# Performance work log

Measured on AMD Instinct MI355X. Metric: run time of the kernel, lower is better.

The kernel has to match this reference:

```python
import jax, jax.numpy as jnp
import numpy as np

B, N, E = 64, 256, 2048          # graphs per batch, nodes per subgraph, edges per subgraph
V, D, H = 50000, 128, 4          # vocab_size, hidden_dim, heads
NEG_SLOPE = 0.2                  # PyG GATConv default LeakyReLU slope


def setup_inputs() -> dict:
    key = jax.random.key(0)
    ks = jax.random.split(key, 16)
    s = 0.05
    return {
        "neighbors_node1": jax.random.randint(ks[0], (B, N), 0, V),
        "neighbors_node2": jax.random.randint(ks[1], (B, N), 0, V),
        "adj1": jax.random.randint(ks[2], (B, 2, E), 0, N),
        "adj2": jax.random.randint(ks[3], (B, 2, E), 0, N),
        "emb": jax.random.normal(ks[4], (V + 1, D), jnp.float32) * 0.02,
        # GATConv 1: lin weight [H*D, D], att_src/att_dst [H, D], bias [D] (concat=False)
        "W1": jax.random.normal(ks[5], (H * D, D), jnp.float32) * s,
        "att_src1": jax.random.normal(ks[6], (H, D), jnp.float32) * s,
        "att_dst1": jax.random.normal(ks[7], (H, D), jnp.float32) * s,
        "b1": jnp.zeros((D,), jnp.float32),
        # GATConv 2
        "W2": jax.random.normal(ks[8], (H * D, D), jnp.float32) * s,
        "att_src2": jax.random.normal(ks[9], (H, D), jnp.float32) * s,
        "att_dst2": jax.random.normal(ks[10], (H, D), jnp.float32) * s,
        "b2": jnp.zeros((D,), jnp.float32),
        # final MLP: Linear(2D -> 1)
        "mlp_w": jax.random.normal(ks[11], (1, 2 * D), jnp.float32) * s,
        "mlp_b": jnp.zeros((1,), jnp.float32),
    }


def _gat_conv(x, edge_index, W, a_src, a_dst, bias):
    """PyG GATConv, concat=False (mean over heads), with self-loops.
    x: [N, D] node features; edge_index: [2, E] (row=src j, col=dst i)."""
    xh = (x @ W.T).reshape(N, H, D)                      # [N, H, D]
    loop = jnp.arange(N)
    src = jnp.concatenate([edge_index[0], loop])          # [E+N]
    dst = jnp.concatenate([edge_index[1], loop])
    asrc = jnp.einsum('nhd,hd->nh', xh, a_src)            # [N, H]
    adst = jnp.einsum('nhd,hd->nh', xh, a_dst)
    e = jax.nn.leaky_relu(asrc[src] + adst[dst], NEG_SLOPE)   # [E+N, H]
    # softmax over incoming edges of each dst node
    m = jax.ops.segment_max(e, dst, num_segments=N)
    ex = jnp.exp(e - m[dst])
    denom = jax.ops.segment_sum(ex, dst, num_segments=N)
    alpha = ex / denom[dst]                               # [E+N, H]
    out = jax.ops.segment_sum(xh[src] * alpha[:, :, None], dst, num_segments=N)  # [N, H, D]
    return out.mean(axis=1) + bias                        # [N, D]


def reference(neighbors_node1, neighbors_node2, adj1, adj2, emb,
              W1, att_src1, att_dst1, b1,
              W2, att_src2, att_dst2, b2,
              mlp_w, mlp_b):
    f1 = jax.vmap(lambda n, ei: _gat_conv(emb[n], ei, W1, att_src1, att_dst1, b1))(
        neighbors_node1, adj1)                            # [B, N, D]
    f2 = jax.vmap(lambda n, ei: _gat_conv(emb[n], ei, W2, att_src2, att_dst2, b2))(
        neighbors_node2, adj2)
    feats = jnp.concatenate([f1[:, 0], f2[:, 0]], axis=-1)  # center node of each subgraph -> [B, 2D]
    return (feats @ mlp_w.T + mlp_b)[:, 0]                # [B]
```

## Files before the change

### kernel.cpp

```cpp
#include <hip/hip_runtime.h>
#include <hip/hip_bf16.h>

#define Bg 64
#define Nn 256
#define Ee 2048
#define Dd 128
#define Hh 4
#define MAXJ 40
#define RS 132

__device__ __forceinline__ float bf2f(unsigned short u) {
    return __uint_as_float(((unsigned)u) << 16);
}

__global__ __launch_bounds__(256) void precompute_kernel(
    const void* W1, const void* as1, const void* ad1, const void* b1,
    const void* W2, const void* as2, const void* ad2, const void* b2,
    const void* mlpw, const void* mlpb, float* wv)
{
    __shared__ float s_av[3 * Dd];
    __shared__ float s_part[8 * 3 * Dd];
    __shared__ float s_red[2];
    __shared__ int   s_f32;

    const int tid = threadIdx.x;
    const int x = blockIdx.x;
    const int l = x >> 2, h = x & 3;

    if (tid < 64) {
        float v = bf2f(((const unsigned short*)W1)[tid]);
        bool bad = !(v > -64.f && v < 64.f);
        unsigned long long m = __ballot(bad);
        if (tid == 0) s_f32 = (m != 0ull) ? 1 : 0;
    }
    __syncthreads();
    const int f32 = s_f32;

    for (int i = tid; i < 3 * Dd; i += 256) {
        int t = i >> 7, d = i & 127;
        const void* p; long off;
        if (t == 0)      { p = l ? as2 : as1; off = (long)h * Dd + d; }
        else if (t == 1) { p = l ? ad2 : ad1; off = (long)h * Dd + d; }
        else             { p = mlpw;          off = (long)l * Dd + d; }
        s_av[i] = f32 ? ((const float*)p)[off]
                      : bf2f(((const unsigned short*)p)[off]);
    }
    __syncthreads();

    {
        const int kc = (tid & 31) * 4;
        const int d0 = (tid >> 5) * 16;
        float acc[3][4] = {};
        if (f32) {
            const float* Wf = (const float*)(l ? W2 : W1) + (long)h * Dd * Dd;
            #pragma unroll
            for (int dd = 0; dd < 16; ++dd) {
                int d = d0 + dd;
                float4 w = *(const float4*)(Wf + (long)d * Dd + kc);
                #pragma unroll
                for (int t = 0; t < 3; ++t) {
                    float a = s_av[t * Dd + d];
                    acc[t][0] += a * w.x; acc[t][1] += a * w.y;
                    acc[t][2] += a * w.z; acc[t][3] += a * w.w;
                }
            }
        } else {
            const unsigned short* Wb =
                (const unsigned short*)(l ? W2 : W1) + (long)h * Dd * Dd;
            #pragma unroll
            for (int dd = 0; dd < 16; ++dd) {
                int d = d0 + dd;
                ushort4 u = *(const ushort4*)(Wb + (long)d * Dd + kc);
                float wx = bf2f(u.x), wy = bf2f(u.y);
                float wz = bf2f(u.z), ww = bf2f(u.w);
                #pragma unroll
                for (int t = 0; t < 3; ++t) {
                    float a = s_av[t * Dd + d];
                    acc[t][0] += a * wx; acc[t][1] += a * wy;
                    acc[t][2] += a * wz; acc[t][3] += a * ww;
                }
            }
        }
        const int dg = tid >> 5;
        #pragma unroll
        for (int t = 0; t < 3; ++t)
            *(float4*)&s_part[(dg * 3 + t) * Dd + kc] =
                make_float4(acc[t][0], acc[t][1], acc[t][2], acc[t][3]);
    }
    __syncthreads();

    for (int i = tid; i < 3 * Dd; i += 256) {
        int t = i >> 7, k = i & 127;
        float s = 0.f;
        #pragma unroll
        for (int g = 0; g < 8; ++g) s += s_part[(g * 3 + t) * Dd + k];
        wv[((l * 3 + t) * 4 + h) * Dd + k] = s;
    }

    if (h == 0) {
        float p = 0.f;
        if (tid < 128) {
            const void* bias = l ? b2 : b1;
            float bv = f32 ? ((const float*)bias)[tid]
                           : bf2f(((const unsigned short*)bias)[tid]);
            p = bv * s_av[2 * Dd + tid];
        }
        #pragma unroll
        for (int off = 32; off > 0; off >>= 1) p += __shfl_down(p, off);
        if (tid == 0 || tid == 64) s_red[tid >> 6] = p;
        __syncthreads();
        if (tid == 0) {
            float a = s_red[0] + s_red[1];
            if (l == 0) a += f32 ? ((const float*)mlpb)[0]
                                 : bf2f(((const unsigned short*)mlpb)[0]);
            wv[3072 + l] = a;
        }
    }
}

__global__ __launch_bounds__(512) void gat_main_kernel(
    const int* nn1, const int* nn2, const int* adj1, const int* adj2,
    const void* emb, const void* W1, const float* wv, void* out)
{
    __shared__ float s_wv[24 * RS];
    __shared__ float s_rows[2 * MAXJ * RS];
    __shared__ int   s_nodes[2][Nn];
    __shared__ int   s_srcj[2][MAXJ];
    __shared__ int   s_gid[2 * MAXJ];
    __shared__ int   s_cnt[2];
    __shared__ int   s_f32;
    __shared__ float s_ps[2 * MAXJ * Hh], s_pm[2 * MAXJ * Hh];
    __shared__ float s_pd[2 * Hh], s_hval[2 * Hh], s_bdot[2];

    const int tid = threadIdx.x;
    const int b = blockIdx.x;

    if (tid == 0) { s_cnt[0] = 0; s_cnt[1] = 0; }
    if (tid < 64) {
        float v = bf2f(((const unsigned short*)W1)[tid]);
        bool bad = !(v > -64.f && v < 64.f);
        unsigned long long m = __ballot(bad);
        if (tid == 0) s_f32 = (m != 0ull) ? 1 : 0;
    }
    __syncthreads();
    const int f32 = s_f32;

    for (int v = tid; v < 2 * (Ee / 4); v += 512) {
        int l = v >> 9, i = v & 511;
        const int* adjp = (l ? adj2 : adj1) + (long)b * 2 * Ee;
        int4 d4 = ((const int4*)(adjp + Ee))[i];
        int base = i * 4;
        if (d4.x == 0) { int p = atomicAdd(&s_cnt[l], 1); if (p < MAXJ - 1) s_srcj[l][p] = adjp[base + 0]; }
        if (d4.y == 0) { int p = atomicAdd(&s_cnt[l], 1); if (p < MAXJ - 1) s_srcj[l][p] = adjp[base + 1]; }
        if (d4.z == 0) { int p = atomicAdd(&s_cnt[l], 1); if (p < MAXJ - 1) s_srcj[l][p] = adjp[base + 2]; }
        if (d4.w == 0) { int p = atomicAdd(&s_cnt[l], 1); if (p < MAXJ - 1) s_srcj[l][p] = adjp[base + 3]; }
    }
    {
        int l = tid >> 8, n = tid & 255;
        s_nodes[l][n] = (l ? nn2 : nn1)[b * Nn + n];
    }
    for (int i = tid; i < 768; i += 512) {
        float4 f = ((const float4*)wv)[i];
        int el = i * 4, row = el >> 7, k = el & 127;
        *(float4*)&s_wv[row * RS + k] = f;
    }
    if (tid < 2) s_bdot[tid] = wv[3072 + tid];
    __syncthreads();

    if (tid < 2) {
        int c = s_cnt[tid];
        if (c > MAXJ - 1) c = MAXJ - 1;
        s_srcj[tid][c] = 0;
        s_cnt[tid] = c + 1;
    }
    __syncthreads();
    const int cnt0 = s_cnt[0], cnt1 = s_cnt[1];
    const int tot = cnt0 + cnt1;

    if (tid < 2 * MAXJ) {
        int l = tid / MAXJ, j = tid % MAXJ;
        int cl = l ? cnt1 : cnt0;
        if (j < cl) s_gid[l ? (cnt0 + j) : j] = s_nodes[l][s_srcj[l][j]];
    }
    __syncthreads();

    if (f32) {
        for (int idx = tid; idx < tot * 32; idx += 512) {
            int j = idx >> 5, k4 = (idx & 31) << 2;
            long gid = s_gid[j];
            float4 f = ((const float4*)emb)[gid * 32 + (k4 >> 2)];
            *(float4*)&s_rows[j * RS + k4] = f;
        }
    } else {
        for (int idx = tid; idx < tot * 16; idx += 512) {
            int j = idx >> 4, k8 = (idx & 15) << 3;
            long gid = s_gid[j];
            uint4 u = *(const uint4*)((const unsigned short*)emb + gid * Dd + k8);
            float4 f0 = make_float4(bf2f(u.x & 0xffff), bf2f(u.x >> 16),
                                    bf2f(u.y & 0xffff), bf2f(u.y >> 16));
            float4 f1 = make_float4(bf2f(u.z & 0xffff), bf2f(u.z >> 16),
                                    bf2f(u.w & 0xffff), bf2f(u.w >> 16));
            *(float4*)&s_rows[j * RS + k8] = f0;
            *(float4*)&s_rows[j * RS + k8 + 4] = f1;
        }
    }
    __syncthreads();

    const int ntask = tot * 8 + 8;
    for (int task = tid; task < ntask; task += 512) {
        int j, h, t, l;
        if (task < tot * 8) {
            j = task >> 3; h = (task >> 1) & 3; t = (task & 1) ? 2 : 0;
            l = (j < cnt0) ? 0 : 1;
        } else {
            int z = task - tot * 8;
            l = z >> 2; h = z & 3; t = 1;
            j = l ? (tot - 1) : (cnt0 - 1);
        }
        const float* wrow = s_wv + ((l * 3 + t) * 4 + h) * RS;
        const float* row  = s_rows + j * RS;
        float acc = 0.f;
        #pragma unroll 8
        for (int k = 0; k < Dd; ++k) acc += row[k] * wrow[k];
        if (task < tot * 8) {
            if (task & 1) s_pm[j * Hh + h] = acc;
            else          s_ps[j * Hh + h] = acc;
        } else {
            s_pd[(l << 2) | h] = acc;
        }
    }
    __syncthreads();

    if (tid < 8) {
        int l = tid >> 2, h = tid & 3;
        int j0 = l ? cnt0 : 0;
        int j1 = l ? tot : cnt0;
        float pd = s_pd[tid], m = -1e30f;
        for (int j = j0; j < j1; ++j) {
            float e = s_ps[j * Hh + h] + pd;
            e = (e >= 0.f) ? e : 0.2f * e;
            s_ps[j * Hh + h] = e;
            if (e > m) m = e;
        }
        float den = 0.f, num = 0.f;
        for (int j = j0; j < j1; ++j) {
            float ex = expf(s_ps[j * Hh + h] - m);
            den += ex;
            num += ex * s_pm[j * Hh + h];
        }
        s_hval[tid] = num / den;
    }
    __syncthreads();
    if (tid == 0) {
        float r = 0.25f * (s_hval[0] + s_hval[1] + s_hval[2] + s_hval[3]) + s_bdot[0]
                + 0.25f * (s_hval[4] + s_hval[5] + s_hval[6] + s_hval[7]) + s_bdot[1];
        if (f32) ((float*)out)[b] = r;
        else     ((__hip_bfloat16*)out)[b] = __float2bfloat16(r);
    }
}

extern "C" void kernel_launch(void* const* d_in, const int* in_sizes, int n_in,
                              void* d_out, int out_size, void* d_ws, size_t ws_size,
                              hipStream_t stream) {
    const int* nn1  = (const int*)d_in[0];
    const int* nn2  = (const int*)d_in[1];
    const int* adj1 = (const int*)d_in[2];
    const int* adj2 = (const int*)d_in[3];
    float* wv = (float*)d_ws;

    precompute_kernel<<<8, 256, 0, stream>>>(
        d_in[5],   d_in[6],   d_in[7],
        d_in[8],
        d_in[9],   d_in[10],  d_in[11],
        d_in[12],
        d_in[13],  d_in[14],  wv);

    gat_main_kernel<<<Bg, 512, 0, stream>>>(
        nn1, nn2, adj1, adj2, d_in[4] , d_in[5] , wv, d_out);
}
```

Measured before the change: 105.2 us.

## Fuse weight-projection precompute into main GAT kernel, recomputing per block

Removes the separate precompute kernel and has every block recompute the attention/MLP vector projections of W1/W2 itself, overlapping that work with the embedding gather. Adjacency loads are issued up front in a single pass per thread instead of in a loop. This drops one kernel launch and the workspace round trip. In exchange, each of the 64 blocks re-reads both full weight matrices (about 512KB) from L2 and does redundant FLOPs.

```diff
diff --git a/kernel.cpp b/kernel.cpp
--- a/kernel.cpp
+++ b/kernel.cpp
@@ -13,129 +13,43 @@
     return __uint_as_float(((unsigned)u) << 16);
 }
 
-__global__ __launch_bounds__(256) void precompute_kernel(
+__global__ __launch_bounds__(512) void gat_fused_kernel(
+    const int* nn1, const int* nn2, const int* adj1, const int* adj2,
+    const void* emb,
     const void* W1, const void* as1, const void* ad1, const void* b1,
     const void* W2, const void* as2, const void* ad2, const void* b2,
-    const void* mlpw, const void* mlpb, float* wv)
-{
-    __shared__ float s_av[3 * Dd];
-    __shared__ float s_part[8 * 3 * Dd];
-    __shared__ float s_red[2];
-    __shared__ int   s_f32;
-
-    const int tid = threadIdx.x;
-    const int x = blockIdx.x;
-    const int l = x >> 2, h = x & 3;
-
-    if (tid < 64) {
-        float v = bf2f(((const unsigned short*)W1)[tid]);
-        bool bad = !(v > -64.f && v < 64.f);
-        unsigned long long m = __ballot(bad);
-        if (tid == 0) s_f32 = (m != 0ull) ? 1 : 0;
-    }
-    __syncthreads();
-    const int f32 = s_f32;
-
-    for (int i = tid; i < 3 * Dd; i += 256) {
-        int t = i >> 7, d = i & 127;
-        const void* p; long off;
-        if (t == 0)      { p = l ? as2 : as1; off = (long)h * Dd + d; }
-        else if (t == 1) { p = l ? ad2 : ad1; off = (long)h * Dd + d; }
-        else             { p = mlpw;          off = (long)l * Dd + d; }
-        s_av[i] = f32 ? ((const float*)p)[off]
-                      : bf2f(((const unsigned short*)p)[off]);
-    }
-    __syncthreads();
-
-    {
-        const int kc = (tid & 31) * 4;
-        const int d0 = (tid >> 5) * 16;
-        float acc[3][4] = {};
-        if (f32) {
-            const float* Wf = (const float*)(l ? W2 : W1) + (long)h * Dd * Dd;
-            #pragma unroll
-            for (int dd = 0; dd < 16; ++dd) {
-                int d = d0 + dd;
-                float4 w = *(const float4*)(Wf + (long)d * Dd + kc);
-                #pragma unroll
-                for (int t = 0; t < 3; ++t) {
-                    float a = s_av[t * Dd + d];
-                    acc[t][0] += a * w.x; acc[t][1] += a * w.y;
-                    acc[t][2] += a * w.z; acc[t][3] += a * w.w;
-                }
-            }
-        } else {
-            const unsigned short* Wb =
-                (const unsigned short*)(l ? W2 : W1) + (long)h * Dd * Dd;
-            #pragma unroll
-            for (int dd = 0; dd < 16; ++dd) {
-                int d = d0 + dd;
-                ushort4 u = *(const ushort4*)(Wb + (long)d * Dd + kc);
-                float wx = bf2f(u.x), wy = bf2f(u.y);
-                float wz = bf2f(u.z), ww = bf2f(u.w);
-                #pragma unroll
-                for (int t = 0; t < 3; ++t) {
-                    float a = s_av[t * Dd + d];
-                    acc[t][0] += a * wx; acc[t][1] += a * wy;
-                    acc[t][2] += a * wz; acc[t][3] += a * ww;
-                }
-            }
-        }
-        const int dg = tid >> 5;
-        #pragma unroll
-        for (int t = 0; t < 3; ++t)
-            *(float4*)&s_part[(dg * 3 + t) * Dd + kc] =
-                make_float4(acc[t][0], acc[t][1], acc[t][2], acc[t][3]);
-    }
-    __syncthreads();
-
-    for (int i = tid; i < 3 * Dd; i += 256) {
-        int t = i >> 7, k = i & 127;
-        float s = 0.f;
-        #pragma unroll
-        for (int g = 0; g < 8; ++g) s += s_part[(g * 3 + t) * Dd + k];
-        wv[((l * 3 + t) * 4 + h) * Dd + k] = s;
-    }
-
-    if (h == 0) {
-        float p = 0.f;
-        if (tid < 128) {
-            const void* bias = l ? b2 : b1;
-            float bv = f32 ? ((const float*)bias)[tid]
-                           : bf2f(((const unsigned short*)bias)[tid]);
-            p = bv * s_av[2 * Dd + tid];
-        }
-        #pragma unroll
-        for (int off = 32; off > 0; off >>= 1) p += __shfl_down(p, off);
-        if (tid == 0 || tid == 64) s_red[tid >> 6] = p;
-        __syncthreads();
-        if (tid == 0) {
-            float a = s_red[0] + s_red[1];
-            if (l == 0) a += f32 ? ((const float*)mlpb)[0]
-                                 : bf2f(((const unsigned short*)mlpb)[0]);
-            wv[3072 + l] = a;
-        }
-    }
-}
-
-__global__ __launch_bounds__(512) void gat_main_kernel(
-    const int* nn1, const int* nn2, const int* adj1, const int* adj2,
-    const void* emb, const void* W1, const float* wv, void* out)
+    const void* mlpw, const void* mlpb, void* out)
 {
     __shared__ float s_wv[24 * RS];
     __shared__ float s_rows[2 * MAXJ * RS];
+    __shared__ float s_att[2 * 2 * Hh * Dd];
+    __shared__ float s_mlp[2 * Dd];
     __shared__ int   s_nodes[2][Nn];
     __shared__ int   s_srcj[2][MAXJ];
     __shared__ int   s_gid[2 * MAXJ];
     __shared__ int   s_cnt[2];
     __shared__ int   s_f32;
     __shared__ float s_ps[2 * MAXJ * Hh], s_pm[2 * MAXJ * Hh];
-    __shared__ float s_pd[2 * Hh], s_hval[2 * Hh], s_bdot[2];
+    __shared__ float s_pd[2 * Hh], s_hval[2 * Hh];
+    __shared__ float s_red4[4];
 
     const int tid = threadIdx.x;
     const int b = blockIdx.x;
 
-    if (tid == 0) { s_cnt[0] = 0; s_cnt[1] = 0; }
+    const int* adjp0 = adj1 + (long)b * 2 * Ee;
+    const int* adjp1 = adj2 + (long)b * 2 * Ee;
+    int4 d0 = ((const int4*)(adjp0 + Ee))[tid];
+    int4 s0 = ((const int4*)adjp0)[tid];
+    int4 d1 = ((const int4*)(adjp1 + Ee))[tid];
+    int4 s1 = ((const int4*)adjp1)[tid];
+
+    {
+        int l = tid >> 8, n = tid & 255;
+        s_nodes[l][n] = (l ? nn2 : nn1)[b * Nn + n];
+    }
+
+    if (tid < 2) s_cnt[tid] = 0;
+
     if (tid < 64) {
         float v = bf2f(((const unsigned short*)W1)[tid]);
         bool bad = !(v > -64.f && v < 64.f);
@@ -145,42 +59,68 @@
     __syncthreads();
     const int f32 = s_f32;
 
-    for (int v = tid; v < 2 * (Ee / 4); v += 512) {
-        int l = v >> 9, i = v & 511;
-        const int* adjp = (l ? adj2 : adj1) + (long)b * 2 * Ee;
-        int4 d4 = ((const int4*)(adjp + Ee))[i];
-        int base = i * 4;
-        if (d4.x == 0) { int p = atomicAdd(&s_cnt[l], 1); if (p < MAXJ - 1) s_srcj[l][p] = adjp[base + 0]; }
-        if (d4.y == 0) { int p = atomicAdd(&s_cnt[l], 1); if (p < MAXJ - 1) s_srcj[l][p] = adjp[base + 1]; }
-        if (d4.z == 0) { int p = atomicAdd(&s_cnt[l], 1); if (p < MAXJ - 1) s_srcj[l][p] = adjp[base + 2]; }
-        if (d4.w == 0) { int p = atomicAdd(&s_cnt[l], 1); if (p < MAXJ - 1) s_srcj[l][p] = adjp[base + 3]; }
-    }
     {
-        int l = tid >> 8, n = tid & 255;
-        s_nodes[l][n] = (l ? nn2 : nn1)[b * Nn + n];
-    }
-    for (int i = tid; i < 768; i += 512) {
-        float4 f = ((const float4*)wv)[i];
-        int el = i * 4, row = el >> 7, k = el & 127;
-        *(float4*)&s_wv[row * RS + k] = f;
-    }
-    if (tid < 2) s_bdot[tid] = wv[3072 + tid];
-    __syncthreads();
-
-    if (tid < 2) {
-        int c = s_cnt[tid];
-        if (c > MAXJ - 1) c = MAXJ - 1;
-        s_srcj[tid][c] = 0;
-        s_cnt[tid] = c + 1;
-    }
-    __syncthreads();
-    const int cnt0 = s_cnt[0], cnt1 = s_cnt[1];
-    const int tot = cnt0 + cnt1;
+        #define SCAN1(c, sv, l) \
+            if ((c) == 0) { int p = atomicAdd(&s_cnt[l], 1); \
+                            if (p < MAXJ - 1) s_srcj[l][p] = (sv); }
+        SCAN1(d0.x, s0.x, 0) SCAN1(d0.y, s0.y, 0)
+        SCAN1(d0.z, s0.z, 0) SCAN1(d0.w, s0.w, 0)
+        SCAN1(d1.x, s1.x, 1) SCAN1(d1.y, s1.y, 1)
+        SCAN1(d1.z, s1.z, 1) SCAN1(d1.w, s1.w, 1)
+        #undef SCAN1
+    }
+
+    for (int i = tid; i < 2304; i += 512) {
+        if (i < 2048) {
+            int l = i >> 10, t = (i >> 9) & 1, h = (i >> 7) & 3, d = i & 127;
+            const void* p = l ? (t ? ad2 : as2) : (t ? ad1 : as1);
+            long off = (long)h * Dd + d;
+            s_att[((l * 2 + t) * Hh + h) * Dd + d] =
+                f32 ? ((const float*)p)[off]
+                    : bf2f(((const unsigned short*)p)[off]);
+        } else {
+            int z = i - 2048, l = z >> 7, d = z & 127;
+            s_mlp[l * Dd + d] =
+                f32 ? ((const float*)mlpw)[l * Dd + d]
+                    : bf2f(((const unsigned short*)mlpw)[l * Dd + d]);
+        }
+    }
+
+    if (tid < 256) {
+        int l = tid >> 7, d = tid & 127;
+        const void* bp = l ? b2 : b1;
+        float bv = f32 ? ((const float*)bp)[d]
+                       : bf2f(((const unsigned short*)bp)[d]);
+        float mv = f32 ? ((const float*)mlpw)[l * Dd + d]
+                       : bf2f(((const unsigned short*)mlpw)[l * Dd + d]);
+        float p = bv * mv;
+        #pragma unroll
+        for (int off = 32; off > 0; off >>= 1) p += __shfl_down(p, off);
+        if ((tid & 63) == 0) s_red4[tid >> 6] = p;
+    }
+    __syncthreads();
+
+    float bd0 = 0.f, bd1 = 0.f;
+    if (tid == 0) {
+        bd0 = s_red4[0] + s_red4[1] +
+              (f32 ? ((const float*)mlpb)[0]
+                   : bf2f(((const unsigned short*)mlpb)[0]));
+        bd1 = s_red4[2] + s_red4[3];
+    }
+
+    int c0 = s_cnt[0]; if (c0 > MAXJ - 1) c0 = MAXJ - 1; c0 += 1;
+    int c1 = s_cnt[1]; if (c1 > MAXJ - 1) c1 = MAXJ - 1; c1 += 1;
+    const int tot = c0 + c1;
 
     if (tid < 2 * MAXJ) {
-        int l = tid / MAXJ, j = tid % MAXJ;
-        int cl = l ? cnt1 : cnt0;
-        if (j < cl) s_gid[l ? (cnt0 + j) : j] = s_nodes[l][s_srcj[l][j]];
+        int l = tid >= MAXJ;
+        int j = l ? tid - MAXJ : tid;
+        int cl = l ? c1 : c0;
+        int base = l ? c0 : 0;
+        if (j < cl) {
+            int src = (j == cl - 1) ? 0 : s_srcj[l][j];
+            s_gid[base + j] = s_nodes[l][src];
+        }
     }
     __syncthreads();
 
@@ -204,6 +144,42 @@
             *(float4*)&s_rows[j * RS + k8 + 4] = f1;
         }
     }
+
+    {
+        const int w = tid >> 6, lane = tid & 63;
+        const int l = w >> 2, h = w & 3;
+        const int k0 = lane * 2;
+        const float* av0 = s_att + ((l * 2 + 0) * Hh + h) * Dd;
+        const float* av1 = s_att + ((l * 2 + 1) * Hh + h) * Dd;
+        const float* av2 = s_mlp + l * Dd;
+        float a00 = 0.f, a01 = 0.f, a10 = 0.f, a11 = 0.f, a20 = 0.f, a21 = 0.f;
+        if (f32) {
+            const float* Wf = (const float*)(l ? W2 : W1) + (long)h * Dd * Dd;
+            #pragma unroll 8
+            for (int d = 0; d < Dd; ++d) {
+                float2 wr = *(const float2*)(Wf + (long)d * Dd + k0);
+                float x0 = av0[d], x1 = av1[d], x2 = av2[d];
+                a00 += x0 * wr.x; a01 += x0 * wr.y;
+                a10 += x1 * wr.x; a11 += x1 * wr.y;
+                a20 += x2 * wr.x; a21 += x2 * wr.y;
+            }
+        } else {
+            const unsigned short* Wb =
+                (const unsigned short*)(l ? W2 : W1) + (long)h * Dd * Dd;
+            #pragma unroll 8
+            for (int d = 0; d < Dd; ++d) {
+                unsigned u = *(const unsigned*)(Wb + (long)d * Dd + k0);
+                float wx = bf2f(u & 0xffff), wy = bf2f(u >> 16);
+                float x0 = av0[d], x1 = av1[d], x2 = av2[d];
+                a00 += x0 * wx; a01 += x0 * wy;
+                a10 += x1 * wx; a11 += x1 * wy;
+                a20 += x2 * wx; a21 += x2 * wy;
+            }
+        }
+        *(float2*)&s_wv[((l * 3 + 0) * Hh + h) * RS + k0] = make_float2(a00, a01);
+        *(float2*)&s_wv[((l * 3 + 1) * Hh + h) * RS + k0] = make_float2(a10, a11);
+        *(float2*)&s_wv[((l * 3 + 2) * Hh + h) * RS + k0] = make_float2(a20, a21);
+    }
     __syncthreads();
 
     const int ntask = tot * 8 + 8;
@@ -211,13 +187,13 @@
         int j, h, t, l;
         if (task < tot * 8) {
             j = task >> 3; h = (task >> 1) & 3; t = (task & 1) ? 2 : 0;
-            l = (j < cnt0) ? 0 : 1;
+            l = (j < c0) ? 0 : 1;
         } else {
             int z = task - tot * 8;
             l = z >> 2; h = z & 3; t = 1;
-            j = l ? (tot - 1) : (cnt0 - 1);
-        }
-        const float* wrow = s_wv + ((l * 3 + t) * 4 + h) * RS;
+            j = l ? (tot - 1) : (c0 - 1);
+        }
+        const float* wrow = s_wv + ((l * 3 + t) * Hh + h) * RS;
         const float* row  = s_rows + j * RS;
         float acc = 0.f;
         #pragma unroll 8
@@ -233,8 +209,8 @@
 
     if (tid < 8) {
         int l = tid >> 2, h = tid & 3;
-        int j0 = l ? cnt0 : 0;
-        int j1 = l ? tot : cnt0;
+        int j0 = l ? c0 : 0;
+        int j1 = l ? tot : c0;
         float pd = s_pd[tid], m = -1e30f;
         for (int j = j0; j < j1; ++j) {
             float e = s_ps[j * Hh + h] + pd;
@@ -252,8 +228,8 @@
     }
     __syncthreads();
     if (tid == 0) {
-        float r = 0.25f * (s_hval[0] + s_hval[1] + s_hval[2] + s_hval[3]) + s_bdot[0]
-                + 0.25f * (s_hval[4] + s_hval[5] + s_hval[6] + s_hval[7]) + s_bdot[1];
+        float r = 0.25f * (s_hval[0] + s_hval[1] + s_hval[2] + s_hval[3]) + bd0
+                + 0.25f * (s_hval[4] + s_hval[5] + s_hval[6] + s_hval[7]) + bd1;
         if (f32) ((float*)out)[b] = r;
         else     ((__hip_bfloat16*)out)[b] = __float2bfloat16(r);
     }
@@ -262,19 +238,15 @@
 extern "C" void kernel_launch(void* const* d_in, const int* in_sizes, int n_in,
                               void* d_out, int out_size, void* d_ws, size_t ws_size,
                               hipStream_t stream) {
-    const int* nn1  = (const int*)d_in[0];
-    const int* nn2  = (const int*)d_in[1];
-    const int* adj1 = (const int*)d_in[2];
-    const int* adj2 = (const int*)d_in[3];
-    float* wv = (float*)d_ws;
-
-    precompute_kernel<<<8, 256, 0, stream>>>(
+    gat_fused_kernel<<<Bg, 512, 0, stream>>>(
+        (const int*)d_in[0],
+        (const int*)d_in[1],
+        (const int*)d_in[2],
+        (const int*)d_in[3],
+        d_in[4],
         d_in[5],   d_in[6],   d_in[7],
         d_in[8],
         d_in[9],   d_in[10],  d_in[11],
         d_in[12],
-        d_in[13],  d_in[14],  wv);
-
-    gat_main_kernel<<<Bg, 512, 0, stream>>>(
-        nn1, nn2, adj1, adj2, d_in[4] , d_in[5] , wv, d_out);
+        d_in[13],  d_in[14],  d_out);
 }
```

Result: slower. 110.5 us (+5.0%).
